# Kernel tuning notes

Measured on AMD Instinct MI355X. Metric: run time of the kernel, lower is better.

The kernel has to match this reference:

```python
import jax, jax.numpy as jnp
import numpy as np

D_MODEL = 1024
N_HEAD = 16
D_K = D_MODEL // N_HEAD
B, S = 4, 2048


def setup_inputs() -> dict:
    key = jax.random.key(0)
    ks = jax.random.split(key, 12)
    def w(k):
        return jax.random.normal(k, (D_MODEL, D_MODEL), dtype=jnp.float32) * 0.02
    def b(k):
        return jax.random.normal(k, (D_MODEL,), dtype=jnp.float32) * 0.02
    return {
        "x": jax.random.normal(ks[0], (B, S, D_MODEL), dtype=jnp.float32),
        "pos_emb": jax.random.normal(ks[1], (S, D_MODEL), dtype=jnp.float32),
        "Wq": w(ks[2]), "bq": b(ks[3]),
        "Wk": w(ks[4]), "bk": b(ks[5]),
        "Wv": w(ks[6]), "bv": b(ks[7]),
        "Wp": w(ks[8]), "bp": b(ks[9]),
        "Wo": w(ks[10]), "bo": b(ks[11]),
    }


def reference(x, pos_emb, Wq, bq, Wk, bk, Wv, bv, Wp, bp, Wo, bo):
    # x: [B, S, D]; pos_emb: [S, D]. cache=None path (prefill): kv_len == S.
    Bsz, Sl, _ = x.shape
    def heads(t):  # [B, S, D] -> [B, H, S, dk]
        return t.reshape(Bsz, Sl, N_HEAD, D_K).transpose(0, 2, 1, 3)
    q = heads(x @ Wq.T + bq)
    k = heads(x @ Wk.T + bk)
    v = heads(x @ Wv.T + bv)
    # pos projection: [S, D] -> [H, S, dk]
    p = (pos_emb @ Wp.T + bp).reshape(Sl, N_HEAD, D_K).transpose(1, 0, 2)
    q_pos = q + p[None]  # broadcast over batch
    scores = jnp.einsum("bhqd,bhkd->bhqk", q_pos, k) / jnp.sqrt(jnp.asarray(D_K, x.dtype))
    # causal mask: triu(ones(S, S), diagonal=1) positions are masked
    causal = jnp.tril(jnp.ones((Sl, Sl), dtype=bool))  # True = keep
    scores = jnp.where(causal[None, None], scores, -jnp.inf)
    attn = jax.nn.softmax(scores, axis=-1)  # dropout is identity (eval / p=0)
    out = jnp.einsum("bhqk,bhkd->bhqd", attn, v)
    out = out.transpose(0, 2, 1, 3).reshape(Bsz, Sl, D_MODEL)
    return out @ Wo.T + bo
```

## Files before the change

### kernel.cpp

```cpp
#include <hip/hip_runtime.h>

#define D_MODEL 1024
#define N_HEADS 16
#define DK 64
#define BATCH 4
#define SEQ 2048
#define MROWS (BATCH * SEQ)
#define TILE_E (256 * 64)

typedef float f32x4 __attribute__((ext_vector_type(4)));
typedef short bf16x8 __attribute__((ext_vector_type(8)));
typedef unsigned short u16;
typedef unsigned short u16x8 __attribute__((ext_vector_type(8)));

__device__ __forceinline__ float bf2f(u16 u) {
    union { unsigned int i; float f; } v; v.i = ((unsigned int)u) << 16; return v.f;
}
__device__ __forceinline__ u16 f2bf(float f) {
    union { float f; unsigned int i; } v; v.f = f;
    unsigned int u = v.i;
    u += 0x7fffu + ((u >> 16) & 1u);
    return (u16)(u >> 16);
}
__device__ __forceinline__ unsigned int pk2(float a, float b) {
    union { float f; unsigned int i; } ua, ub; ua.f = a; ub.f = b;
    return __builtin_amdgcn_perm(ub.i + 0x8000u, ua.i + 0x8000u, 0x07060302u);
}

typedef unsigned int u32_as1 __attribute__((address_space(1)));
typedef unsigned int u32_as3 __attribute__((address_space(3)));
__device__ __forceinline__ void gload16(const u16* g, u16* l) {
    __builtin_amdgcn_global_load_lds((const u32_as1*)g, (u32_as3*)l, 16, 0, 0);
}

__global__ __launch_bounds__(256) void convert_all(
    const float* __restrict__ x, const float* __restrict__ pe,
    const float* __restrict__ w0, const float* __restrict__ w1, const float* __restrict__ w2,
    const float* __restrict__ w3, const float* __restrict__ w4,
    u16* __restrict__ xb, u16* __restrict__ pb,
    u16* __restrict__ wb0, u16* __restrict__ wb1, u16* __restrict__ wb2,
    u16* __restrict__ wb3, u16* __restrict__ wb4)
{
    int t = blockIdx.x * 256 + threadIdx.x;
    const float* src; u16* dst; int idx;
    if (t < 1048576)      { src = x;  dst = xb; idx = t; }
    else if (t < 1310720) { src = pe; dst = pb; idx = t - 1048576; }
    else {
        int r = t - 1310720; int w = r >> 17; idx = r & 131071;
        if      (w == 0) { src = w0; dst = wb0; }
        else if (w == 1) { src = w1; dst = wb1; }
        else if (w == 2) { src = w2; dst = wb2; }
        else if (w == 3) { src = w3; dst = wb3; }
        else             { src = w4; dst = wb4; }
    }
    const float4* p = (const float4*)src + (size_t)idx * 2;
    float4 a = p[0], b = p[1];
    u16x8 o;
    o[0] = f2bf(a.x); o[1] = f2bf(a.y); o[2] = f2bf(a.z); o[3] = f2bf(a.w);
    o[4] = f2bf(b.x); o[5] = f2bf(b.y); o[6] = f2bf(b.z); o[7] = f2bf(b.w);
    *((u16x8*)dst + idx) = o;
}

#define SA(bufp, h, kk) do { \
    gload16(Ag + (size_t)((h) * 64) * 1024 + (kk),       (bufp) + ((h) * 64 + wv * 8) * 64); \
    gload16(Ag + (size_t)((h) * 64 + 128) * 1024 + (kk), (bufp) + ((h) * 64 + 128 + wv * 8) * 64); \
} while (0)
#define SB(bufp, h, kk) do { \
    gload16(Wg + (size_t)((h) * 32) * 1024 + (kk),       (bufp) + (wq2 * 64 + (h) * 32 + w3 * 8) * 64); \
    gload16(Wg + (size_t)((h) * 32 + 128) * 1024 + (kk), (bufp) + (128 + wq2 * 64 + (h) * 32 + w3 * 8) * 64); \
} while (0)
#define LOAD_A(mh) \
    _Pragma("unroll") \
    for (int mi = 0; mi < 4; ++mi) { \
        aA[mi][0] = *(const bf16x8*)&Abuf[aoff0 + ((mh) * 64 + mi * 16) * 64]; \
        aA[mi][1] = *(const bf16x8*)&Abuf[aoff1 + ((mh) * 64 + mi * 16) * 64]; \
    }
#define LOAD_B(nh) \
    _Pragma("unroll") \
    for (int ni = 0; ni < 2; ++ni) { \
        bB[nh][ni][0] = *(const bf16x8*)&Bbuf[boff0 + ((nh) * 32 + ni * 16) * 64]; \
        bB[nh][ni][1] = *(const bf16x8*)&Bbuf[boff1 + ((nh) * 32 + ni * 16) * 64]; \
    }
#define MFMA16(mh, nh) \
    _Pragma("unroll") \
    for (int ks = 0; ks < 2; ++ks) \
        _Pragma("unroll") \
        for (int mi = 0; mi < 4; ++mi) \
            _Pragma("unroll") \
            for (int ni = 0; ni < 2; ++ni) \
                acc[(mh) * 4 + mi][(nh) * 2 + ni] = __builtin_amdgcn_mfma_f32_16x16x32_bf16( \
                    aA[mi][ks], bB[nh][ni][ks], acc[(mh) * 4 + mi][(nh) * 2 + ni], 0, 0, 0);

__device__ __forceinline__ void gemm256_loop(
    const u16* __restrict__ Ag, const u16* __restrict__ Wg,
    u16* AsBase, u16* BsBase, int wv,
    int aoff0, int aoff1, int boff0, int boff1, f32x4 (&acc)[8][4])
{
    const int wq2 = wv >> 2, w3 = wv & 3;
    bf16x8 aA[4][2], bB[2][2][2];

    SA(AsBase, 0, 0); SB(BsBase, 0, 0); SB(BsBase, 1, 0); SA(AsBase, 1, 0);
    SA(AsBase + TILE_E, 0, 64); SB(BsBase + TILE_E, 0, 64); SA(AsBase + TILE_E, 1, 64);
    asm volatile("s_waitcnt vmcnt(6)" ::: "memory");
    __builtin_amdgcn_s_barrier();

    for (int T = 0; T < 16; ++T) {
        u16* Abuf = AsBase + (T & 1) * TILE_E;
        u16* Bbuf = BsBase + (T & 1) * TILE_E;
        u16* Both = BsBase + ((T & 1) ^ 1) * TILE_E;
        const int k2 = T * 64 + 128;

        LOAD_A(0); LOAD_B(0);
        if (T < 15) SB(Both, 1, T * 64 + 64);
        __builtin_amdgcn_s_barrier();
        asm volatile("s_waitcnt lgkmcnt(0)" ::: "memory");
        __builtin_amdgcn_s_setprio(1); MFMA16(0, 0); __builtin_amdgcn_s_setprio(0);
        __builtin_amdgcn_s_barrier();

        LOAD_B(1);
        if (T < 14) SA(Abuf, 0, k2);
        __builtin_amdgcn_s_barrier();
        asm volatile("s_waitcnt lgkmcnt(0)" ::: "memory");
        __builtin_amdgcn_s_setprio(1); MFMA16(0, 1); __builtin_amdgcn_s_setprio(0);
        __builtin_amdgcn_s_barrier();

        LOAD_A(1);
        if (T < 14) SB(Bbuf, 0, k2);
        __builtin_amdgcn_s_barrier();
        asm volatile("s_waitcnt lgkmcnt(0)" ::: "memory");
        __builtin_amdgcn_s_setprio(1); MFMA16(1, 0); __builtin_amdgcn_s_setprio(0);
        __builtin_amdgcn_s_barrier();

        if (T < 14) SA(Abuf, 1, k2);
        __builtin_amdgcn_s_barrier();
        __builtin_amdgcn_s_setprio(1); MFMA16(1, 1); __builtin_amdgcn_s_setprio(0);
        if (T < 14)      { asm volatile("s_waitcnt vmcnt(6)" ::: "memory"); }
        else if (T < 15) { asm volatile("s_waitcnt vmcnt(0)" ::: "memory"); }
        __builtin_amdgcn_s_barrier();
    }
}

__global__ __launch_bounds__(512, 2) void qkv_gemm256(
    const u16* __restrict__ xb, const u16* __restrict__ peb,
    const u16* __restrict__ wqb, const u16* __restrict__ wkb,
    const u16* __restrict__ wvb, const u16* __restrict__ wpb,
    const float* __restrict__ bq, const float* __restrict__ bk,
    const float* __restrict__ bv, const float* __restrict__ bp,
    u16* __restrict__ Qb, u16* __restrict__ Kb, u16* __restrict__ V3,
    u16* __restrict__ Pb)
{
    __shared__ __align__(16) u16 SH[4 * TILE_E];
    u16* As = SH;
    u16* Bs = SH + 2 * TILE_E;

    const int tid  = threadIdx.x;
    const int lane = tid & 63;
    const int wv   = tid >> 6;
    const int l15  = lane & 15;
    const int quad = lane >> 4;
    const int wm = wv >> 2, wn = wv & 3;

    int wg = (blockIdx.x & 7) * 52 + (blockIdx.x >> 3);
    int chunk, m0, n0;
    if (wg < 384) {
        int g = wg >> 5;
        chunk = g >> 2; n0 = (g & 3) * 256; m0 = (wg & 31) * 256;
    } else {
        int r = wg - 384;
        chunk = 3; n0 = (r >> 3) * 256; m0 = (r & 7) * 256;
    }

    const u16* Abase = (chunk == 3) ? peb : xb;
    const u16* Wbase = (chunk == 0) ? wqb : ((chunk == 1) ? wkb : ((chunk == 2) ? wvb : wpb));

    const int trow = tid >> 3;
    const int swz  = ((tid & 7) ^ (trow & 7)) * 8;
    const u16* Ag = Abase + (size_t)(m0 + trow) * 1024 + swz;
    const u16* Wg = Wbase + (size_t)(n0 + (wv >> 2) * 64 + (trow & 31)) * 1024 + swz;

    const int x7 = l15 & 7;
    const int aoff0 = (wm * 128 + l15) * 64 + ((quad    ) ^ x7) * 8;
    const int aoff1 = (wm * 128 + l15) * 64 + ((quad + 4) ^ x7) * 8;
    const int boff0 = (wn * 64 + l15) * 64 + ((quad    ) ^ x7) * 8;
    const int boff1 = (wn * 64 + l15) * 64 + ((quad + 4) ^ x7) * 8;

    f32x4 acc[8][4];
#pragma unroll
    for (int i = 0; i < 8; ++i)
#pragma unroll
        for (int j = 0; j < 4; ++j) acc[i][j] = f32x4{0.f, 0.f, 0.f, 0.f};

    gemm256_loop(Ag, Wg, As, Bs, wv, aoff0, aoff1, boff0, boff1, acc);

    const float* bias = (chunk == 0) ? bq : ((chunk == 1) ? bk : ((chunk == 2) ? bv : bp));
    const int r0 = quad * 4;
    if (chunk == 2) {
#pragma unroll
        for (int n = 0; n < 4; ++n) {
            int col = n0 + wn * 64 + n * 16 + l15;
            float bvv = bias[col];
#pragma unroll
            for (int m = 0; m < 8; ++m) {
                int row0 = m0 + wm * 128 + m * 16 + r0;
                int hh = col >> 6, d = col & 63;
                int bb = row0 >> 11, sl = row0 & 2047;
                union { u16 h[4]; uint2 v; } pk;
#pragma unroll
                for (int r = 0; r < 4; ++r) pk.h[r] = f2bf(acc[m][n][r] + bvv);
                *((uint2*)V3 + ((size_t)(bb * 16 + hh) * 512 + (sl >> 2)) * 64 + d) = pk.v;
            }
        }
    } else {
        u16* dst = (chunk == 0) ? Qb : ((chunk == 1) ? Kb : Pb);
#pragma unroll
        for (int p = 0; p < 2; ++p) {
            __syncthreads();
            if (wm == p) {
#pragma unroll
                for (int n = 0; n < 4; ++n) {
                    int colL = wn * 64 + n * 16 + l15;
                    float bvv = bias[n0 + colL];
#pragma unroll
                    for (int m = 0; m < 8; ++m) {
#pragma unroll
                        for (int r = 0; r < 4; ++r)
                            SH[(m * 16 + r0 + r) * 264 + colL] = f2bf(acc[m][n][r] + bvv);
                    }
                }
            }
            __syncthreads();
            const int rbase = m0 + p * 128;
#pragma unroll
            for (int s = 0; s < 2; ++s) {
                int rowL = (tid >> 3) + s * 64;
#pragma unroll
                for (int i = 0; i < 4; ++i) {
                    int cc = (tid & 7) + i * 8;
                    *(u16x8*)(dst + (size_t)(rbase + rowL) * 1024 + n0 + cc * 8) =
                        *(const u16x8*)&SH[rowL * 264 + cc * 8];
                }
            }
        }
    }
}

#undef SA
#undef SB
#undef LOAD_A
#undef LOAD_B
#undef MFMA16

__global__ __launch_bounds__(256) void gemm_out(
    const u16* __restrict__ A, const u16* __restrict__ W,
    const float* __restrict__ bias, float* __restrict__ Cout)
{
    __shared__ __align__(16) u16 As[128 * 32];
    __shared__ __align__(16) u16 Bs[128 * 32];

    const int tid  = threadIdx.x;
    const int lane = tid & 63;
    const int wv   = tid >> 6;
    const int l15  = lane & 15;
    const int quad = lane >> 4;
    const int m0   = blockIdx.x * 128;
    const int n0   = blockIdx.y * 128;
    const int wrow = (wv >> 1) * 64;
    const int wcol = (wv & 1) * 64;

    f32x4 acc[4][4];
#pragma unroll
    for (int i = 0; i < 4; ++i)
#pragma unroll
        for (int j = 0; j < 4; ++j) acc[i][j] = f32x4{0.f, 0.f, 0.f, 0.f};

    const int lr = lane >> 2;
    const int lc = (lane & 3) * 8;
    const u16* Ag = A + (size_t)(m0 + wv * 16 + lr) * 1024 + lc;
    const u16* Wg = W + (size_t)(n0 + wv * 16 + lr) * 1024 + lc;
    u16* Al = &As[wv * 16 * 32];
    u16* Bl = &Bs[wv * 16 * 32];

    for (int k0 = 0; k0 < 1024; k0 += 32) {
        __syncthreads();
        gload16(Ag + k0, Al);
        gload16(Ag + 64 * 1024 + k0, Al + 64 * 32);
        gload16(Wg + k0, Bl);
        gload16(Wg + 64 * 1024 + k0, Bl + 64 * 32);
        __syncthreads();

        bf16x8 af[4], bfr[4];
#pragma unroll
        for (int i = 0; i < 4; ++i)
            af[i] = *(const bf16x8*)&As[(wrow + 16 * i + l15) * 32 + quad * 8];
#pragma unroll
        for (int j = 0; j < 4; ++j)
            bfr[j] = *(const bf16x8*)&Bs[(wcol + 16 * j + l15) * 32 + quad * 8];
#pragma unroll
        for (int i = 0; i < 4; ++i)
#pragma unroll
            for (int j = 0; j < 4; ++j)
                acc[i][j] = __builtin_amdgcn_mfma_f32_16x16x32_bf16(af[i], bfr[j], acc[i][j], 0, 0, 0);
    }

    const int r0 = quad * 4;
#pragma unroll
    for (int i = 0; i < 4; ++i)
#pragma unroll
        for (int j = 0; j < 4; ++j) {
            int col = n0 + wcol + 16 * j + l15;
            float bvv = bias[col];
#pragma unroll
            for (int r = 0; r < 4; ++r) {
                int row = m0 + wrow + 16 * i + r0 + r;
                Cout[(size_t)row * 1024 + col] = acc[i][j][r] + bvv;
            }
        }
}

__global__ __launch_bounds__(256, 4) void flash_attn_mfma(
    const u16* __restrict__ Q, const u16* __restrict__ Kq,
    const u16* __restrict__ V3, const u16* __restrict__ Pb, u16* __restrict__ O)
{
    __shared__ __align__(16) u16 Ks[2][64 * 72];
    __shared__ __align__(16) u16 Vs[2][64 * 72];

    const int tid  = threadIdx.x;
    const int lane = tid & 63;
    const int wv   = tid >> 6;
    const int l15  = lane & 15;
    const int quad = lane >> 4;
    const int gg   = blockIdx.x;
    const int h    = gg & 15;
    const int b    = gg >> 4;
    const int y    = 15 - (int)blockIdx.y;
    const int wq0  = y * 128 + wv * 32;
    const int NT   = 2 * y + 2;

    bf16x8 qf[2][2];
    const size_t qrowbase = (size_t)(b * SEQ) * D_MODEL + h * DK;
#pragma unroll
    for (int qb = 0; qb < 2; ++qb)
#pragma unroll
        for (int ks = 0; ks < 2; ++ks) {
            int qrow = wq0 + qb * 16 + l15;
            u16x8 qr = *(const u16x8*)(Q + qrowbase + (size_t)qrow * D_MODEL + ks * 32 + quad * 8);
            u16x8 pr = *(const u16x8*)(Pb + (size_t)qrow * D_MODEL + h * DK + ks * 32 + quad * 8);
            u16x8 o;
#pragma unroll
            for (int t = 0; t < 8; ++t)
                o[t] = f2bf((bf2f(qr[t]) + bf2f(pr[t])) * 0.180336880111120f);
            qf[qb][ks] = *(bf16x8*)&o;
        }

    f32x4 Oacc[2][4];
#pragma unroll
    for (int i = 0; i < 2; ++i)
#pragma unroll
        for (int jj = 0; jj < 4; ++jj) Oacc[i][jj] = f32x4{0.f, 0.f, 0.f, 0.f};
    float l_r[2] = {0.f, 0.f};

    const int sr  = tid >> 2;
    const int sc8 = (tid & 3) * 16;
    const u16* Kg = Kq + (size_t)(b * SEQ + sr) * D_MODEL + h * DK + sc8;

    const uint2* Vgp = (const uint2*)V3 + (size_t)gg * 32768 + tid;
    const int vd = tid & 63;
    int vb[4];
#pragma unroll
    for (int i = 0; i < 4; ++i) {
        int g16 = (tid >> 6) + 4 * i;
        vb[i] = (g16 >> 3) * 32 + (g16 & 3) * 8 + ((g16 >> 2) & 1) * 4;
    }

    u16x8 kr0 = *(const u16x8*)Kg;
    u16x8 kr1 = *(const u16x8*)(Kg + 8);
    uint2 vr0 = Vgp[0], vr1 = Vgp[256], vr2 = Vgp[512], vr3 = Vgp[768];

    *(u16x8*)&Ks[0][sr * 72 + sc8]     = kr0;
    *(u16x8*)&Ks[0][sr * 72 + sc8 + 8] = kr1;
    *(uint2*)&Vs[0][vd * 72 + vb[0]] = vr0;
    *(uint2*)&Vs[0][vd * 72 + vb[1]] = vr1;
    *(uint2*)&Vs[0][vd * 72 + vb[2]] = vr2;
    *(uint2*)&Vs[0][vd * 72 + vb[3]] = vr3;
    __syncthreads();

    for (int kt = 0; kt < NT; ++kt) {
        const int cur = kt & 1;
        if (kt + 1 < NT) {
            const u16* Kn = Kg + (size_t)(kt + 1) * 64 * D_MODEL;
            kr0 = *(const u16x8*)Kn;
            kr1 = *(const u16x8*)(Kn + 8);
            vr0 = Vgp[(size_t)(kt + 1) * 1024];
            vr1 = Vgp[(size_t)(kt + 1) * 1024 + 256];
            vr2 = Vgp[(size_t)(kt + 1) * 1024 + 512];
            vr3 = Vgp[(size_t)(kt + 1) * 1024 + 768];
        }

        if (kt * 64 <= wq0 + 31) {
            f32x4 sacc[4][2];
#pragma unroll
            for (int kb = 0; kb < 4; ++kb)
#pragma unroll
                for (int qb = 0; qb < 2; ++qb) sacc[kb][qb] = f32x4{0.f, 0.f, 0.f, 0.f};
            __builtin_amdgcn_s_setprio(1);
#pragma unroll
            for (int ks = 0; ks < 2; ++ks) {
                bf16x8 kf[4];
#pragma unroll
                for (int kb = 0; kb < 4; ++kb)
                    kf[kb] = *(const bf16x8*)&Ks[cur][(kb * 16 + l15) * 72 + ks * 32 + quad * 8];
#pragma unroll
                for (int kb = 0; kb < 4; ++kb)
#pragma unroll
                    for (int qb = 0; qb < 2; ++qb)
                        sacc[kb][qb] = __builtin_amdgcn_mfma_f32_16x16x32_bf16(kf[kb], qf[qb][ks], sacc[kb][qb], 0, 0, 0);
            }
            __builtin_amdgcn_s_setprio(0);

            if (kt * 64 + 63 > wq0) {
#pragma unroll
                for (int kb = 0; kb < 4; ++kb) {
                    int key_g = kt * 64 + kb * 16 + quad * 4;
#pragma unroll
                    for (int qb = 0; qb < 2; ++qb) {
                        int q_g = wq0 + qb * 16 + l15;
#pragma unroll
                        for (int r = 0; r < 4; ++r)
                            if (key_g + r > q_g) sacc[kb][qb][r] = -1e30f;
                    }
                }
            }

            bf16x8 pf[2][2];
#pragma unroll
            for (int qb = 0; qb < 2; ++qb) {
                float s = 0.f;
                float p[4][4];
#pragma unroll
                for (int kb = 0; kb < 4; ++kb) {
                    p[kb][0] = __builtin_amdgcn_exp2f(sacc[kb][qb][0]);
                    p[kb][1] = __builtin_amdgcn_exp2f(sacc[kb][qb][1]);
                    p[kb][2] = __builtin_amdgcn_exp2f(sacc[kb][qb][2]);
                    p[kb][3] = __builtin_amdgcn_exp2f(sacc[kb][qb][3]);
                    s += (p[kb][0] + p[kb][1]) + (p[kb][2] + p[kb][3]);
                }
                l_r[qb] += s;
#pragma unroll
                for (int ks = 0; ks < 2; ++ks) {
                    union { unsigned int w[4]; bf16x8 v; } u;
                    u.w[0] = pk2(p[2 * ks][0],     p[2 * ks][1]);
                    u.w[1] = pk2(p[2 * ks][2],     p[2 * ks][3]);
                    u.w[2] = pk2(p[2 * ks + 1][0], p[2 * ks + 1][1]);
                    u.w[3] = pk2(p[2 * ks + 1][2], p[2 * ks + 1][3]);
                    pf[qb][ks] = u.v;
                }
            }

            __builtin_amdgcn_s_setprio(1);
#pragma unroll
            for (int ks = 0; ks < 2; ++ks) {
                bf16x8 vf[4];
#pragma unroll
                for (int db = 0; db < 4; ++db)
                    vf[db] = *(const bf16x8*)&Vs[cur][(db * 16 + l15) * 72 + ks * 32 + quad * 8];
#pragma unroll
                for (int qb = 0; qb < 2; ++qb)
#pragma unroll
                    for (int db = 0; db < 4; ++db)
                        Oacc[qb][db] = __builtin_amdgcn_mfma_f32_16x16x32_bf16(pf[qb][ks], vf[db], Oacc[qb][db], 0, 0, 0);
            }
            __builtin_amdgcn_s_setprio(0);
        }

        if (kt + 1 < NT) {
            *(u16x8*)&Ks[cur ^ 1][sr * 72 + sc8]     = kr0;
            *(u16x8*)&Ks[cur ^ 1][sr * 72 + sc8 + 8] = kr1;
            *(uint2*)&Vs[cur ^ 1][vd * 72 + vb[0]] = vr0;
            *(uint2*)&Vs[cur ^ 1][vd * 72 + vb[1]] = vr1;
            *(uint2*)&Vs[cur ^ 1][vd * 72 + vb[2]] = vr2;
            *(uint2*)&Vs[cur ^ 1][vd * 72 + vb[3]] = vr3;
        }
        __syncthreads();
    }

    float linv[2];
#pragma unroll
    for (int qb = 0; qb < 2; ++qb) {
        float s = l_r[qb];
        s += __shfl_xor(s, 16);
        s += __shfl_xor(s, 32);
        linv[qb] = 1.f / s;
    }
#pragma unroll
    for (int qb = 0; qb < 2; ++qb)
#pragma unroll
        for (int r = 0; r < 4; ++r) {
            float li = __shfl(linv[qb], quad * 4 + r);
            size_t row = (size_t)(b * SEQ + wq0 + qb * 16 + quad * 4 + r) * D_MODEL + h * DK;
#pragma unroll
            for (int db = 0; db < 4; ++db)
                O[row + db * 16 + l15] = f2bf(Oacc[qb][db][r] * li);
        }
}

extern "C" void kernel_launch(void* const* d_in, const int* in_sizes, int n_in,
                              void* d_out, int out_size, void* d_ws, size_t ws_size,
                              hipStream_t stream) {
    const float* x  = (const float*)d_in[0];
    const float* pe = (const float*)d_in[1];
    const float* Wq = (const float*)d_in[2];  const float* bq = (const float*)d_in[3];
    const float* Wk = (const float*)d_in[4];  const float* bk = (const float*)d_in[5];
    const float* Wv = (const float*)d_in[6];  const float* bv = (const float*)d_in[7];
    const float* Wp = (const float*)d_in[8];  const float* bp = (const float*)d_in[9];
    const float* Wo = (const float*)d_in[10]; const float* bo = (const float*)d_in[11];
    float* out = (float*)d_out;
    char* ws = (char*)d_ws;

    size_t off = 0;
    u16* xb  = (u16*)(ws + off); off += (size_t)MROWS * D_MODEL * 2;
    u16* peb = (u16*)(ws + off); off += (size_t)SEQ * D_MODEL * 2;
    u16* wqb = (u16*)(ws + off); off += (size_t)D_MODEL * D_MODEL * 2;
    u16* wkb = (u16*)(ws + off); off += (size_t)D_MODEL * D_MODEL * 2;
    u16* wvb = (u16*)(ws + off); off += (size_t)D_MODEL * D_MODEL * 2;
    u16* wpb = (u16*)(ws + off); off += (size_t)D_MODEL * D_MODEL * 2;
    u16* wob = (u16*)(ws + off); off += (size_t)D_MODEL * D_MODEL * 2;
    u16* Qb  = (u16*)(ws + off); off += (size_t)MROWS * D_MODEL * 2;
    u16* Kb  = (u16*)(ws + off); off += (size_t)MROWS * D_MODEL * 2;
    u16* V3b = (u16*)(ws + off); off += (size_t)MROWS * D_MODEL * 2;
    u16* Pb  = (u16*)(ws + off); off += (size_t)SEQ * D_MODEL * 2;
    u16* AO = xb;

    convert_all<<<7680, 256, 0, stream>>>(x, pe, Wq, Wk, Wv, Wp, Wo,
                                          xb, peb, wqb, wkb, wvb, wpb, wob);

    qkv_gemm256<<<416, 512, 0, stream>>>(
        xb, peb, wqb, wkb, wvb, wpb, bq, bk, bv, bp, Qb, Kb, V3b, Pb);

    flash_attn_mfma<<<dim3(64, 16), 256, 0, stream>>>(Qb, Kb, V3b, Pb, AO);

    gemm_out<<<dim3(64, 8), 256, 0, stream>>>(AO, wob, bo, out);
}
```

Before: 260.7 us.

## Replace output GEMM with double-buffered 256x128 pipelined kernel; use hardware bf16 pack

The output projection GEMM moves from a single-buffered 128x128 tile with two barriers per 32-wide K step to a 256x128 tile, 512 threads, K=64 steps, double-buffered LDS, XOR-swizzled layout, and staged global-to-LDS loads that overlap with MFMA phases. Block indices are remapped for locality. The aim is to hide load latency and reduce LDS bank conflicts and sync overhead. Separately, the softmax probability packing in attention uses v_cvt_pk_bf16_f32 instead of the add-and-permute packing.

```diff
diff --git a/kernel.cpp b/kernel.cpp
--- a/kernel.cpp
+++ b/kernel.cpp
@@ -25,6 +25,11 @@
 __device__ __forceinline__ unsigned int pk2(float a, float b) {
     union { float f; unsigned int i; } ua, ub; ua.f = a; ub.f = b;
     return __builtin_amdgcn_perm(ub.i + 0x8000u, ua.i + 0x8000u, 0x07060302u);
+}
+__device__ __forceinline__ unsigned int cvtpk(float a, float b) {
+    unsigned int r;
+    asm("v_cvt_pk_bf16_f32 %0, %1, %2" : "=v"(r) : "v"(a), "v"(b));
+    return r;
 }
 
 typedef unsigned int u32_as1 __attribute__((address_space(1)));
@@ -250,72 +255,134 @@
 #undef LOAD_B
 #undef MFMA16
 
-__global__ __launch_bounds__(256) void gemm_out(
+#define A_TILE (256 * 64)
+#define B_TILE (128 * 64)
+#define SAo(bufp, h, kk) do { \
+    gload16(Ag + (size_t)((h) * 32) * 1024 + (kk),     (bufp) + (adst + (h) * 32) * 64); \
+    gload16(Ag + (size_t)((h) * 32 + 8) * 1024 + (kk), (bufp) + (adst + (h) * 32 + 8) * 64); \
+} while (0)
+#define SBo(bufp, nh, kk) \
+    gload16(Wg + (size_t)((nh) * 32) * 1024 + (kk), (bufp) + (bdst + (nh) * 32) * 64)
+#define LAo(mh) \
+    _Pragma("unroll") \
+    for (int mi = 0; mi < 2; ++mi) { \
+        aA[mi][0] = *(const bf16x8*)&Abuf[aoff0 + ((mh) * 32 + mi * 16) * 64]; \
+        aA[mi][1] = *(const bf16x8*)&Abuf[aoff1 + ((mh) * 32 + mi * 16) * 64]; \
+    }
+#define LBo(nh) \
+    _Pragma("unroll") \
+    for (int ni = 0; ni < 2; ++ni) { \
+        bB[nh][ni][0] = *(const bf16x8*)&Bbuf[boff0 + ((nh) * 32 + ni * 16) * 64]; \
+        bB[nh][ni][1] = *(const bf16x8*)&Bbuf[boff1 + ((nh) * 32 + ni * 16) * 64]; \
+    }
+#define MMo(mh, nh) \
+    _Pragma("unroll") \
+    for (int ks = 0; ks < 2; ++ks) \
+        _Pragma("unroll") \
+        for (int mi = 0; mi < 2; ++mi) \
+            _Pragma("unroll") \
+            for (int ni = 0; ni < 2; ++ni) \
+                acc[(mh) * 2 + mi][(nh) * 2 + ni] = __builtin_amdgcn_mfma_f32_16x16x32_bf16( \
+                    aA[mi][ks], bB[nh][ni][ks], acc[(mh) * 2 + mi][(nh) * 2 + ni], 0, 0, 0);
+
+__global__ __launch_bounds__(512, 2) void gemm_out256n(
     const u16* __restrict__ A, const u16* __restrict__ W,
     const float* __restrict__ bias, float* __restrict__ Cout)
 {
-    __shared__ __align__(16) u16 As[128 * 32];
-    __shared__ __align__(16) u16 Bs[128 * 32];
+    __shared__ __align__(16) u16 As[2 * A_TILE];
+    __shared__ __align__(16) u16 Bs[2 * B_TILE];
 
     const int tid  = threadIdx.x;
     const int lane = tid & 63;
     const int wv   = tid >> 6;
     const int l15  = lane & 15;
     const int quad = lane >> 4;
-    const int m0   = blockIdx.x * 128;
-    const int n0   = blockIdx.y * 128;
-    const int wrow = (wv >> 1) * 64;
-    const int wcol = (wv & 1) * 64;
+    const int wm = wv >> 1, wn = wv & 1;
+
+    int wg = (blockIdx.x & 7) * 32 + (blockIdx.x >> 3);
+    const int m0 = (wg >> 3) * 256;
+    const int n0 = (wg & 7) * 128;
+
+    const int swz    = ((tid & 7) ^ ((tid >> 3) & 7)) * 8;
+    const int arow_t = (wv >> 1) * 64 + (wv & 1) * 16 + (lane >> 3);
+    const int brow_t = (wv >> 2) * 64 + (wv & 3) * 8 + (lane >> 3);
+    const u16* Ag = A + (size_t)(m0 + arow_t) * 1024 + swz;
+    const u16* Wg = W + (size_t)(n0 + brow_t) * 1024 + swz;
+    const int adst = (wv >> 1) * 64 + (wv & 1) * 16;
+    const int bdst = (wv >> 2) * 64 + (wv & 3) * 8;
+
+    const int x7 = l15 & 7;
+    const int aoff0 = (wm * 64 + l15) * 64 + ((quad    ) ^ x7) * 8;
+    const int aoff1 = (wm * 64 + l15) * 64 + ((quad + 4) ^ x7) * 8;
+    const int boff0 = (wn * 64 + l15) * 64 + ((quad    ) ^ x7) * 8;
+    const int boff1 = (wn * 64 + l15) * 64 + ((quad + 4) ^ x7) * 8;
 
     f32x4 acc[4][4];
 #pragma unroll
     for (int i = 0; i < 4; ++i)
 #pragma unroll
         for (int j = 0; j < 4; ++j) acc[i][j] = f32x4{0.f, 0.f, 0.f, 0.f};
-
-    const int lr = lane >> 2;
-    const int lc = (lane & 3) * 8;
-    const u16* Ag = A + (size_t)(m0 + wv * 16 + lr) * 1024 + lc;
-    const u16* Wg = W + (size_t)(n0 + wv * 16 + lr) * 1024 + lc;
-    u16* Al = &As[wv * 16 * 32];
-    u16* Bl = &Bs[wv * 16 * 32];
-
-    for (int k0 = 0; k0 < 1024; k0 += 32) {
-        __syncthreads();
-        gload16(Ag + k0, Al);
-        gload16(Ag + 64 * 1024 + k0, Al + 64 * 32);
-        gload16(Wg + k0, Bl);
-        gload16(Wg + 64 * 1024 + k0, Bl + 64 * 32);
-        __syncthreads();
-
-        bf16x8 af[4], bfr[4];
-#pragma unroll
-        for (int i = 0; i < 4; ++i)
-            af[i] = *(const bf16x8*)&As[(wrow + 16 * i + l15) * 32 + quad * 8];
-#pragma unroll
-        for (int j = 0; j < 4; ++j)
-            bfr[j] = *(const bf16x8*)&Bs[(wcol + 16 * j + l15) * 32 + quad * 8];
-#pragma unroll
-        for (int i = 0; i < 4; ++i)
-#pragma unroll
-            for (int j = 0; j < 4; ++j)
-                acc[i][j] = __builtin_amdgcn_mfma_f32_16x16x32_bf16(af[i], bfr[j], acc[i][j], 0, 0, 0);
+    bf16x8 aA[2][2], bB[2][2][2];
+
+    SAo(As, 0, 0); SBo(Bs, 0, 0); SBo(Bs, 1, 0); SAo(As, 1, 0);
+    SAo(As + A_TILE, 0, 64); SBo(Bs + B_TILE, 0, 64); SAo(As + A_TILE, 1, 64);
+    asm volatile("s_waitcnt vmcnt(5)" ::: "memory");
+    __builtin_amdgcn_s_barrier();
+
+    for (int T = 0; T < 16; ++T) {
+        u16* Abuf = As + (T & 1) * A_TILE;
+        u16* Bbuf = Bs + (T & 1) * B_TILE;
+        u16* Both = Bs + ((T & 1) ^ 1) * B_TILE;
+        const int k2 = T * 64 + 128;
+
+        LAo(0); LBo(0);
+        if (T < 15) SBo(Both, 1, T * 64 + 64);
+        __builtin_amdgcn_s_barrier();
+        asm volatile("s_waitcnt lgkmcnt(0)" ::: "memory");
+        __builtin_amdgcn_s_setprio(1); MMo(0, 0); __builtin_amdgcn_s_setprio(0);
+        __builtin_amdgcn_s_barrier();
+
+        LBo(1);
+        if (T < 14) SAo(Abuf, 0, k2);
+        __builtin_amdgcn_s_barrier();
+        asm volatile("s_waitcnt lgkmcnt(0)" ::: "memory");
+        __builtin_amdgcn_s_setprio(1); MMo(0, 1); __builtin_amdgcn_s_setprio(0);
+        __builtin_amdgcn_s_barrier();
+
+        LAo(1);
+        if (T < 14) SBo(Bbuf, 0, k2);
+        __builtin_amdgcn_s_barrier();
+        asm volatile("s_waitcnt lgkmcnt(0)" ::: "memory");
+        __builtin_amdgcn_s_setprio(1); MMo(1, 0); __builtin_amdgcn_s_setprio(0);
+        __builtin_amdgcn_s_barrier();
+
+        if (T < 14) SAo(Abuf, 1, k2);
+        __builtin_amdgcn_s_barrier();
+        __builtin_amdgcn_s_setprio(1); MMo(1, 1); __builtin_amdgcn_s_setprio(0);
+        if (T < 14)      { asm volatile("s_waitcnt vmcnt(5)" ::: "memory"); }
+        else if (T < 15) { asm volatile("s_waitcnt vmcnt(0)" ::: "memory"); }
+        __builtin_amdgcn_s_barrier();
     }
 
     const int r0 = quad * 4;
 #pragma unroll
-    for (int i = 0; i < 4; ++i)
-#pragma unroll
-        for (int j = 0; j < 4; ++j) {
-            int col = n0 + wcol + 16 * j + l15;
-            float bvv = bias[col];
-#pragma unroll
-            for (int r = 0; r < 4; ++r) {
-                int row = m0 + wrow + 16 * i + r0 + r;
-                Cout[(size_t)row * 1024 + col] = acc[i][j][r] + bvv;
-            }
-        }
-}
+    for (int b2 = 0; b2 < 4; ++b2) {
+        int col = n0 + wn * 64 + (b2 >> 1) * 32 + (b2 & 1) * 16 + l15;
+        float bvv = bias[col];
+#pragma unroll
+        for (int a = 0; a < 4; ++a) {
+            int row0 = m0 + wm * 64 + (a >> 1) * 32 + (a & 1) * 16 + r0;
+#pragma unroll
+            for (int r = 0; r < 4; ++r)
+                Cout[(size_t)(row0 + r) * 1024 + col] = acc[a][b2][r] + bvv;
+        }
+    }
+}
+#undef SAo
+#undef SBo
+#undef LAo
+#undef LBo
+#undef MMo
 
 __global__ __launch_bounds__(256, 4) void flash_attn_mfma(
     const u16* __restrict__ Q, const u16* __restrict__ Kq,
@@ -448,10 +515,10 @@
 #pragma unroll
                 for (int ks = 0; ks < 2; ++ks) {
                     union { unsigned int w[4]; bf16x8 v; } u;
-                    u.w[0] = pk2(p[2 * ks][0],     p[2 * ks][1]);
-                    u.w[1] = pk2(p[2 * ks][2],     p[2 * ks][3]);
-                    u.w[2] = pk2(p[2 * ks + 1][0], p[2 * ks + 1][1]);
-                    u.w[3] = pk2(p[2 * ks + 1][2], p[2 * ks + 1][3]);
+                    u.w[0] = cvtpk(p[2 * ks][0],     p[2 * ks][1]);
+                    u.w[1] = cvtpk(p[2 * ks][2],     p[2 * ks][3]);
+                    u.w[2] = cvtpk(p[2 * ks + 1][0], p[2 * ks + 1][1]);
+                    u.w[3] = cvtpk(p[2 * ks + 1][2], p[2 * ks + 1][3]);
                     pf[qb][ks] = u.v;
                 }
             }
@@ -538,5 +605,5 @@
 
     flash_attn_mfma<<<dim3(64, 16), 256, 0, stream>>>(Qb, Kb, V3b, Pb, AO);
 
-    gemm_out<<<dim3(64, 8), 256, 0, stream>>>(AO, wob, bo, out);
-}
+    gemm_out256n<<<256, 512, 0, stream>>>(AO, wob, bo, out);
+}
```

New measurement: 257.7 us. About the same (-1.1%).
